# Kernel optimization log

Measured on AMD Instinct MI355X. Metric: run time of the kernel, lower is better.

The kernel has to match this reference:

```python
import jax, jax.numpy as jnp
import numpy as np

B, C, H, W = 4, 64, 128, 128
D_INNER, D_STATE, DT_RANK, K = 192, 16, 6, 4  # d_model = 3*C//2 = 96, expand = 2
EPS = 1e-5


def _haar():
    # pywt db1: dec_lo=[s,s], dec_hi=[-s,s]; code reverses dec_* and uses rec_* in
    # original order -> for Haar both dec and rec filter banks are identical.
    s = np.float32(1.0 / np.sqrt(2.0))
    lo = np.array([s, s], np.float32)
    hi = np.array([s, -s], np.float32)
    # stack order: [lo(i)lo(j), hi(i)lo(j), lo(i)hi(j), hi(i)hi(j)]
    return np.stack([np.outer(lo, lo), np.outer(hi, lo),
                     np.outer(lo, hi), np.outer(hi, hi)], 0)  # (4,2,2)

DEC = jnp.asarray(_haar())
REC = jnp.asarray(_haar())
DN = ('NCHW', 'OIHW', 'NCHW')


def _ln(x, s, b):
    m = x.mean(-1, keepdims=True)
    v = x.var(-1, keepdims=True)
    return (x - m) * jax.lax.rsqrt(v + EPS) * s + b


def _wt(x):
    b, c, h, w = x.shape
    wf = jnp.tile(DEC[:, None], (c, 1, 1, 1))  # (4c,1,2,2), groups=c, pad=0 for db1
    y = jax.lax.conv_general_dilated(x, wf, (2, 2), 'VALID',
                                     feature_group_count=c, dimension_numbers=DN)
    return y.reshape(b, c, 4, h // 2, w // 2)


def _iwt(x):
    # conv_transpose2d(stride=2, pad=0, groups=c) == lhs-dilated conv with flipped kernel, pad k-1
    b, c = x.shape[0], x.shape[1]
    h2, w2 = x.shape[3], x.shape[4]
    xr = x.reshape(b, c * 4, h2, w2)
    wf = jnp.tile(REC[:, ::-1, ::-1][None], (c, 1, 1, 1))  # (c,4,2,2)
    return jax.lax.conv_general_dilated(xr, wf, (1, 1), ((1, 1), (1, 1)),
                                        lhs_dilation=(2, 2), feature_group_count=c,
                                        dimension_numbers=DN)


def _ss2d(x, in_proj_w, conv_dw_w, conv_dw_b, x_proj_w, dt_proj_w, dt_proj_b,
          A_log, Ds, out_norm_s, out_norm_b, out_proj_w):
    b, d, h, w = x.shape  # d == D_INNER
    L = h * w
    xz = jnp.einsum('bchw,ec->behw', x, in_proj_w)  # (b,2d,h,w)
    x1, z = xz[:, :d], xz[:, d:]
    x1 = jax.lax.conv_general_dilated(x1, conv_dw_w, (1, 1), ((1, 1), (1, 1)),
                                      feature_group_count=d, dimension_numbers=DN)
    x1 = jax.nn.silu(x1 + conv_dw_b[None, :, None, None])
    # 4-direction flattening: hw, wh, and their reverses
    xf = x1.reshape(b, d, L)
    xt = x1.transpose(0, 1, 3, 2).reshape(b, d, L)
    xs = jnp.stack([xf, xt], 1)
    xs = jnp.concatenate([xs, xs[..., ::-1]], 1)  # (b,K,d,L)
    x_dbl = jnp.einsum('bkdl,kcd->bkcl', xs, x_proj_w)
    dts = x_dbl[:, :, :DT_RANK]
    Bs = x_dbl[:, :, DT_RANK:DT_RANK + D_STATE]   # (b,K,n,L)
    Cs = x_dbl[:, :, DT_RANK + D_STATE:]
    delta = jax.nn.softplus(jnp.einsum('bkrl,kdr->bkdl', dts, dt_proj_w)
                            + dt_proj_b[None, :, :, None])
    A = -jnp.exp(A_log)  # (K,d,n)

    def step(hc, inp):
        d_t, u_t, b_t, c_t = inp  # (b,K,d),(b,K,d),(b,K,n),(b,K,n)
        dA = jnp.exp(d_t[..., None] * A[None])
        hc = hc * dA + (d_t * u_t)[..., None] * b_t[:, :, None, :]
        y = jnp.einsum('bkdn,bkn->bkd', hc, c_t)
        return hc, y

    h0 = jnp.zeros((b, K, d, D_STATE), x.dtype)
    inputs = (delta.transpose(3, 0, 1, 2), xs.transpose(3, 0, 1, 2),
              Bs.transpose(3, 0, 1, 2), Cs.transpose(3, 0, 1, 2))
    _, ys = jax.lax.scan(step, h0, inputs)            # (L,b,K,d)
    out_y = ys.transpose(1, 2, 3, 0) + xs * Ds[None, :, :, None]  # (b,K,d,L)
    inv_y = out_y[:, 2:][..., ::-1]
    wh = out_y[:, 1].reshape(b, d, w, h).transpose(0, 1, 3, 2).reshape(b, d, L)
    invwh = inv_y[:, 1].reshape(b, d, w, h).transpose(0, 1, 3, 2).reshape(b, d, L)
    y = out_y[:, 0] + inv_y[:, 0] + wh + invwh        # (b,d,L)
    y = _ln(y.reshape(b, d, h, w).transpose(0, 2, 3, 1), out_norm_s, out_norm_b)
    y = y * jax.nn.silu(z.transpose(0, 2, 3, 1))
    y = jnp.einsum('bhwd,ed->bhwe', y, out_proj_w)
    return y.transpose(0, 3, 1, 2)


def reference(x, wt_low_scale, wt_high_scale, low_conv_w, in_proj_w, conv_dw_w,
              conv_dw_b, x_proj_w, dt_proj_w, dt_proj_b, A_log, Ds,
              out_norm_s, out_norm_b, out_proj_w, ln2_s, ln2_b, eca_w):
    b, c = x.shape[0], x.shape[1]
    wt = _wt(x)                                       # (b,c,4,h2,w2)
    h2, w2 = wt.shape[3], wt.shape[4]
    low = wt[:, :, 0] * wt_low_scale
    high = wt[:, :, 1:].reshape(b, c * 3, h2, w2) * wt_high_scale
    low = jax.nn.silu(jnp.einsum('bchw,ec->behw', low, low_conv_w[:, :, 0, 0]))
    high = _ss2d(high, in_proj_w, conv_dw_w, conv_dw_b, x_proj_w, dt_proj_w,
                 dt_proj_b, A_log, Ds, out_norm_s, out_norm_b, out_proj_w)
    high = _ln(high.transpose(0, 2, 3, 1), ln2_s, ln2_b).transpose(0, 3, 1, 2)
    mamba = jnp.tile(low, (1, 3, 1, 1)) * high
    merged = jnp.concatenate([low, mamba], 1).reshape(b, c, 4, h2, w2)
    y = _iwt(merged)                                  # (b,c,h,w)
    # ECA: gap -> conv1d(k=5) over channels -> sigmoid gate
    pooled = y.mean((2, 3))[:, None, :]               # (b,1,c)
    att = jax.lax.conv_general_dilated(pooled, eca_w.reshape(1, 1, 5), (1,),
                                       ((2, 2),), dimension_numbers=('NCH', 'OIH', 'NCH'))
    att = jax.nn.sigmoid(att[:, 0])
    return y * att[:, :, None, None] + x


def setup_inputs():
    key = jax.random.key(0)
    ks = jax.random.split(key, 20)
    f = jax.random.normal
    return {
        'x': f(ks[0], (B, C, H, W), jnp.float32),
        'wt_low_scale': jax.random.uniform(ks[1], (1, C, 1, 1), jnp.float32),
        'wt_high_scale': jax.random.uniform(ks[2], (1, 3 * C, 1, 1), jnp.float32),
        'low_conv_w': f(ks[3], (C, C, 1, 1), jnp.float32) * 0.1,
        'in_proj_w': f(ks[4], (2 * D_INNER, D_INNER), jnp.float32) * 0.05,
        'conv_dw_w': f(ks[5], (D_INNER, 1, 3, 3), jnp.float32) * 0.3,
        'conv_dw_b': f(ks[6], (D_INNER,), jnp.float32) * 0.1,
        'x_proj_w': f(ks[7], (K, DT_RANK + 2 * D_STATE, D_INNER), jnp.float32) * 0.05,
        'dt_proj_w': f(ks[8], (K, D_INNER, DT_RANK), jnp.float32) * 0.1,
        'dt_proj_b': jax.random.uniform(ks[9], (K, D_INNER), jnp.float32) - 4.0,
        'A_log': jax.random.uniform(ks[10], (K, D_INNER, D_STATE), jnp.float32),
        'Ds': f(ks[11], (K, D_INNER), jnp.float32) * 0.1,
        'out_norm_s': jnp.ones((D_INNER,), jnp.float32),
        'out_norm_b': jnp.zeros((D_INNER,), jnp.float32),
        'out_proj_w': f(ks[12], (D_INNER, D_INNER), jnp.float32) * 0.05,
        'ln2_s': jnp.ones((3 * C,), jnp.float32),
        'ln2_b': jnp.zeros((3 * C,), jnp.float32),
        'eca_w': f(ks[13], (5,), jnp.float32) * 0.3,
    }
```

## Files before the change

### kernel.cpp

```cpp
#include <hip/hip_runtime.h>

constexpr int cB = 4, cC = 64, cH = 128, cW = 128;
constexpr int cL = 4096;
constexpr int cD = 192, cN = 16;
constexpr int NCH = 64, CHUNK = 64;

__device__ __forceinline__ float silu_f(float v) { return v / (1.f + __expf(-v)); }

__global__ __launch_bounds__(256) void k_wt(const float* __restrict__ x,
                                            const float* __restrict__ wls,
                                            const float* __restrict__ whs,
                                            float* __restrict__ lraw,
                                            float* __restrict__ high) {
    int idx = blockIdx.x * 256 + threadIdx.x;
    int j = idx & 63, i = (idx >> 6) & 63, c = (idx >> 12) & 63, b = idx >> 18;
    const float* xp = x + (((size_t)(b * cC + c)) * cH + 2 * i) * cW + 2 * j;
    float x00 = xp[0], x01 = xp[1], x10 = xp[cW], x11 = xp[cW + 1];
    float s0 = 0.5f * (x00 + x01 + x10 + x11);
    float s1 = 0.5f * (x00 + x01 - x10 - x11);
    float s2 = 0.5f * (x00 - x01 + x10 - x11);
    float s3 = 0.5f * (x00 - x01 - x10 + x11);
    int l = i * 64 + j;
    lraw[(size_t)(b * cC + c) * cL + l] = s0 * wls[c];
    int ch = c * 3;
    high[(size_t)(b * cD + ch + 0) * cL + l] = s1 * whs[ch + 0];
    high[(size_t)(b * cD + ch + 1) * cL + l] = s2 * whs[ch + 1];
    high[(size_t)(b * cD + ch + 2) * cL + l] = s3 * whs[ch + 2];
}

__global__ __launch_bounds__(256) void k_lowconv(const float* __restrict__ lraw,
                                                 const float* __restrict__ w,
                                                 float* __restrict__ lowT) {
    int bid = blockIdx.x;
    int lt0 = (bid & 63) * 64;
    int b = bid >> 6;
    __shared__ float sW[16][68];
    __shared__ float sI[16][65];
    int tid = threadIdx.x, lt = tid & 63, eg = tid >> 6;
    float acc[16];
#pragma unroll
    for (int m = 0; m < 16; m++) acc[m] = 0.f;
    for (int c0 = 0; c0 < 64; c0 += 16) {
#pragma unroll
        for (int q = 0; q < 4; q++) {
            int tt = tid + q * 256;
            int cc = tt & 15, ee = tt >> 4;
            sW[cc][ee] = w[ee * 64 + c0 + cc];
        }
#pragma unroll
        for (int q = 0; q < 4; q++) {
            int tt = tid + q * 256;
            int ll = tt & 63, cc = tt >> 6;
            sI[cc][ll] = lraw[(size_t)(b * cC + c0 + cc) * cL + lt0 + ll];
        }
        __syncthreads();
#pragma unroll
        for (int cc = 0; cc < 16; cc++) {
            float iv = sI[cc][lt];
#pragma unroll
            for (int m = 0; m < 16; m++) acc[m] = fmaf(sW[cc][eg * 16 + m], iv, acc[m]);
        }
        __syncthreads();
    }
#pragma unroll
    for (int m = 0; m < 16; m++) {
        int e = eg * 16 + m;
        lowT[((size_t)b * cL + lt0 + lt) * 64 + e] = silu_f(acc[m]);
    }
}

__global__ __launch_bounds__(256) void k_inproj(const float* __restrict__ hi,
                                                const float* __restrict__ w,
                                                float* __restrict__ xout,
                                                float* __restrict__ zT) {
    int bid = blockIdx.x;
    int lt0 = (bid & 63) * 64;
    int et = (bid >> 6) % 6;
    int b = bid / (6 * 64);
    int e0 = et * 64;
    __shared__ float sW[16][68];
    __shared__ float sI[16][65];
    int tid = threadIdx.x, lt = tid & 63, eg = tid >> 6;
    float acc[16];
#pragma unroll
    for (int m = 0; m < 16; m++) acc[m] = 0.f;
    for (int c0 = 0; c0 < 192; c0 += 16) {
#pragma unroll
        for (int q = 0; q < 4; q++) {
            int tt = tid + q * 256;
            int cc = tt & 15, ee = tt >> 4;
            sW[cc][ee] = w[(e0 + ee) * 192 + c0 + cc];
        }
#pragma unroll
        for (int q = 0; q < 4; q++) {
            int tt = tid + q * 256;
            int ll = tt & 63, cc = tt >> 6;
            sI[cc][ll] = hi[(size_t)(b * cD + c0 + cc) * cL + lt0 + ll];
        }
        __syncthreads();
#pragma unroll
        for (int cc = 0; cc < 16; cc++) {
            float iv = sI[cc][lt];
#pragma unroll
            for (int m = 0; m < 16; m++) acc[m] = fmaf(sW[cc][eg * 16 + m], iv, acc[m]);
        }
        __syncthreads();
    }
#pragma unroll
    for (int m = 0; m < 16; m++) {
        int e = e0 + eg * 16 + m;
        float v = acc[m];
        if (e < 192) xout[(size_t)(b * cD + e) * cL + lt0 + lt] = v;
        else zT[((size_t)b * cL + lt0 + lt) * 192 + (e - 192)] = v;
    }
}

__global__ __launch_bounds__(256) void k_dwconv(const float* __restrict__ xin,
                                                const float* __restrict__ w,
                                                const float* __restrict__ bias,
                                                float* __restrict__ x1,
                                                float* __restrict__ u1) {
    int bd = blockIdx.x;
    int d = bd % cD;
    const float* xp = xin + (size_t)bd * cL;
    float wv[9];
#pragma unroll
    for (int t = 0; t < 9; t++) wv[t] = w[d * 9 + t];
    float bv = bias[d];
    __shared__ float sm[64][65];
    int tid = threadIdx.x;
#pragma unroll
    for (int q = 0; q < 16; q++) {
        int p = tid + q * 256;
        int i = p >> 6, j = p & 63;
        float acc = bv;
#pragma unroll
        for (int di = 0; di < 3; di++) {
            int ii = i + di - 1;
            if (ii < 0 || ii >= 64) continue;
#pragma unroll
            for (int dj = 0; dj < 3; dj++) {
                int jj = j + dj - 1;
                if (jj < 0 || jj >= 64) continue;
                acc = fmaf(wv[di * 3 + dj], xp[ii * 64 + jj], acc);
            }
        }
        sm[i][j] = silu_f(acc);
    }
    __syncthreads();
#pragma unroll
    for (int q = 0; q < 16; q++) {
        int p = tid + q * 256;
        x1[(size_t)bd * cL + p] = sm[p >> 6][p & 63];
        u1[(size_t)bd * cL + p] = sm[p & 63][p >> 6];
    }
}

__global__ __launch_bounds__(256) void k_xproj(const float* __restrict__ x1,
                                               const float* __restrict__ u1,
                                               const float* __restrict__ xpw,
                                               float* __restrict__ xdbl) {
    int bid = blockIdx.x;
    int lt0 = (bid & 63) * 64;
    int k = (bid >> 6) & 3;
    int b = bid >> 8;
    const float* src = (k & 1) ? u1 : x1;
    bool rev = (k >= 2);
    __shared__ float sW[16][68];
    __shared__ float sI[16][65];
    int tid = threadIdx.x, lt = tid & 63, eg = tid >> 6;
    float acc[16];
#pragma unroll
    for (int m = 0; m < 16; m++) acc[m] = 0.f;
    for (int c0 = 0; c0 < 192; c0 += 16) {
#pragma unroll
        for (int q = 0; q < 4; q++) {
            int tt = tid + q * 256;
            int cc = tt & 15, ee = tt >> 4;
            sW[cc][ee] = (ee < 38) ? xpw[(k * 38 + ee) * 192 + c0 + cc] : 0.f;
        }
#pragma unroll
        for (int q = 0; q < 4; q++) {
            int tt = tid + q * 256;
            int ll = tt & 63, cc = tt >> 6;
            int l = lt0 + ll;
            int lm = rev ? (cL - 1 - l) : l;
            sI[cc][ll] = src[(size_t)(b * cD + c0 + cc) * cL + lm];
        }
        __syncthreads();
#pragma unroll
        for (int cc = 0; cc < 16; cc++) {
            float iv = sI[cc][lt];
#pragma unroll
            for (int m = 0; m < 16; m++) acc[m] = fmaf(sW[cc][eg * 16 + m], iv, acc[m]);
        }
        __syncthreads();
    }
#pragma unroll
    for (int m = 0; m < 16; m++) {
        int e = eg * 16 + m;
        if (e < 38) xdbl[(size_t)((b * 4 + k) * 38 + e) * cL + lt0 + lt] = acc[m];
    }
}

__global__ __launch_bounds__(192) void k_scan1(const float* __restrict__ xdbl,
                                               const float* __restrict__ x1,
                                               const float* __restrict__ u1,
                                               const float* __restrict__ dtw,
                                               const float* __restrict__ dtb,
                                               const float* __restrict__ alog,
                                               float* __restrict__ P,
                                               float* __restrict__ S) {
    int bid = blockIdx.x;
    int ch = bid % NCH;
    int bk = bid / NCH;
    int k = bk & 3, b = bk >> 2;
    int d = threadIdx.x;
    float Av2[16], h[16], Pe[16];
#pragma unroll
    for (int n = 0; n < 16; n++) {
        Av2[n] = -__expf(alog[(k * 192 + d) * 16 + n]) * 1.44269504088896f;
        h[n] = 0.f;
        Pe[n] = 0.f;
    }
    float dtbv = dtb[k * 192 + d];
    float dtwv[6];
#pragma unroll
    for (int r = 0; r < 6; r++) dtwv[r] = dtw[(k * 192 + d) * 6 + r];
    const float* dtrows = xdbl + (size_t)(bk * 38) * cL;
    const float* Brow = xdbl + (size_t)(bk * 38 + 6) * cL;
    const float* usrc = ((k & 1) ? u1 : x1) + (size_t)b * cD * cL;
    bool rev = (k >= 2);

    __shared__ float su[192][17];
    __shared__ float sB[16][16];
    __shared__ float sdt[16][8];

    int col = d & 15, grp = d >> 4;
    int p0 = ch * CHUNK;
    for (int t0 = p0; t0 < p0 + CHUNK; t0 += 16) {
#pragma unroll
        for (int pp = 0; pp < 16; pp++) {
            int row = pp * 12 + grp;
            su[row][col] = usrc[(size_t)row * cL + (rev ? (cL - 1 - (t0 + col)) : (t0 + col))];
        }
        for (int idx = d; idx < 256; idx += 192) {
            sB[idx & 15][idx >> 4] = Brow[(size_t)(idx >> 4) * cL + t0 + (idx & 15)];
        }
        if (d < 96) sdt[col][grp] = dtrows[(size_t)grp * cL + t0 + col];
        __syncthreads();
#pragma unroll
        for (int l = 0; l < 16; l++) {
            float uv = su[d][l];
            float acc = dtbv;
#pragma unroll
            for (int r = 0; r < 6; r++) acc = fmaf(dtwv[r], sdt[l][r], acc);
            float sp = fmaxf(acc, 0.f) + __logf(1.f + __expf(-fabsf(acc)));
            float duB = sp * uv;
            float Bv[16];
            *reinterpret_cast<float4*>(&Bv[0])  = *reinterpret_cast<const float4*>(&sB[l][0]);
            *reinterpret_cast<float4*>(&Bv[4])  = *reinterpret_cast<const float4*>(&sB[l][4]);
            *reinterpret_cast<float4*>(&Bv[8])  = *reinterpret_cast<const float4*>(&sB[l][8]);
            *reinterpret_cast<float4*>(&Bv[12]) = *reinterpret_cast<const float4*>(&sB[l][12]);
#pragma unroll
            for (int n = 0; n < 16; n++) {
                float e = sp * Av2[n];
                Pe[n] += e;
                float dA = exp2f(e);
                h[n] = fmaf(h[n], dA, duB * Bv[n]);
            }
        }
        __syncthreads();
    }
    size_t base = (size_t)bid * 16 * 192 + d;
#pragma unroll
    for (int n = 0; n < 16; n++) {
        P[base + (size_t)n * 192] = exp2f(Pe[n]);
        S[base + (size_t)n * 192] = h[n];
    }
}

__global__ __launch_bounds__(256) void k_carry(const float* __restrict__ P,
                                               float* __restrict__ S) {
    int gid = blockIdx.x * 256 + threadIdx.x;
    int d = gid % 192;
    int n = (gid / 192) & 15;
    int bk = gid / 3072;
    float h = 0.f;
    for (int c = 0; c < NCH; c++) {
        size_t idx = ((size_t)(bk * NCH + c) * 16 + n) * 192 + d;
        h = fmaf(P[idx], h, S[idx]);
        S[idx] = h;
    }
}

__global__ __launch_bounds__(192) void k_scan2(const float* __restrict__ xdbl,
                                               const float* __restrict__ x1,
                                               const float* __restrict__ u1,
                                               const float* __restrict__ dtw,
                                               const float* __restrict__ dtb,
                                               const float* __restrict__ alog,
                                               const float* __restrict__ dss,
                                               const float* __restrict__ S,
                                               float* __restrict__ yacc) {
    int bid = blockIdx.x;
    int ch = bid % NCH;
    int bk = bid / NCH;
    int k = bk & 3, b = bk >> 2;
    int d = threadIdx.x;
    float Av2[16], h[16];
#pragma unroll
    for (int n = 0; n < 16; n++) {
        Av2[n] = -__expf(alog[(k * 192 + d) * 16 + n]) * 1.44269504088896f;
        h[n] = (ch == 0) ? 0.f : S[((size_t)(bk * NCH + ch - 1) * 16 + n) * 192 + d];
    }
    float Dv = dss[k * 192 + d];
    float dtbv = dtb[k * 192 + d];
    float dtwv[6];
#pragma unroll
    for (int r = 0; r < 6; r++) dtwv[r] = dtw[(k * 192 + d) * 6 + r];
    const float* dtrows = xdbl + (size_t)(bk * 38) * cL;
    const float* Brow = xdbl + (size_t)(bk * 38 + 6) * cL;
    const float* Crow = xdbl + (size_t)(bk * 38 + 22) * cL;
    const float* usrc = ((k & 1) ? u1 : x1) + (size_t)b * cD * cL;
    bool rev = (k >= 2);

    __shared__ float su[192][17];
    __shared__ float sB[16][16];
    __shared__ float sC[16][16];
    __shared__ float sdt[16][8];

    int col = d & 15, grp = d >> 4;
    int p0 = ch * CHUNK;
    for (int t0 = p0; t0 < p0 + CHUNK; t0 += 16) {
#pragma unroll
        for (int pp = 0; pp < 16; pp++) {
            int row = pp * 12 + grp;
            su[row][col] = usrc[(size_t)row * cL + (rev ? (cL - 1 - (t0 + col)) : (t0 + col))];
        }
        for (int idx = d; idx < 256; idx += 192) {
            sB[idx & 15][idx >> 4] = Brow[(size_t)(idx >> 4) * cL + t0 + (idx & 15)];
            sC[idx & 15][idx >> 4] = Crow[(size_t)(idx >> 4) * cL + t0 + (idx & 15)];
        }
        if (d < 96) sdt[col][grp] = dtrows[(size_t)grp * cL + t0 + col];
        __syncthreads();
#pragma unroll
        for (int l = 0; l < 16; l++) {
            float uv = su[d][l];
            float acc = dtbv;
#pragma unroll
            for (int r = 0; r < 6; r++) acc = fmaf(dtwv[r], sdt[l][r], acc);
            float sp = fmaxf(acc, 0.f) + __logf(1.f + __expf(-fabsf(acc)));
            float duB = sp * uv;
            float Bv[16], Cv[16];
            *reinterpret_cast<float4*>(&Bv[0])  = *reinterpret_cast<const float4*>(&sB[l][0]);
            *reinterpret_cast<float4*>(&Bv[4])  = *reinterpret_cast<const float4*>(&sB[l][4]);
            *reinterpret_cast<float4*>(&Bv[8])  = *reinterpret_cast<const float4*>(&sB[l][8]);
            *reinterpret_cast<float4*>(&Bv[12]) = *reinterpret_cast<const float4*>(&sB[l][12]);
            *reinterpret_cast<float4*>(&Cv[0])  = *reinterpret_cast<const float4*>(&sC[l][0]);
            *reinterpret_cast<float4*>(&Cv[4])  = *reinterpret_cast<const float4*>(&sC[l][4]);
            *reinterpret_cast<float4*>(&Cv[8])  = *reinterpret_cast<const float4*>(&sC[l][8]);
            *reinterpret_cast<float4*>(&Cv[12]) = *reinterpret_cast<const float4*>(&sC[l][12]);
            float y = uv * Dv;
#pragma unroll
            for (int n = 0; n < 16; n++) {
                float dA = exp2f(sp * Av2[n]);
                h[n] = fmaf(h[n], dA, duB * Bv[n]);
                y = fmaf(h[n], Cv[n], y);
            }
            int lg = t0 + l;
            int lm;
            if (k == 0) lm = lg;
            else if (k == 1) lm = (lg & 63) * 64 + (lg >> 6);
            else if (k == 2) lm = cL - 1 - lg;
            else { int q = cL - 1 - lg; lm = (q & 63) * 64 + (q >> 6); }
            atomicAdd(&yacc[((size_t)b * cL + lm) * 192 + d], y);
        }
        __syncthreads();
    }
}

__global__ __launch_bounds__(256) void k_comb(const float* __restrict__ yacc,
                                              const float* __restrict__ zT,
                                              const float* __restrict__ ons,
                                              const float* __restrict__ onb,
                                              float* __restrict__ yln) {
    int bid = blockIdx.x;
    int b = bid >> 10;
    int pg = bid & 1023;
    int tid = threadIdx.x;
    int wq = tid >> 6, lane = tid & 63;
    int l = pg * 4 + wq;
    float v[3];
    float s = 0.f, s2 = 0.f;
#pragma unroll
    for (int m = 0; m < 3; m++) {
        int d = lane + 64 * m;
        float t = yacc[((size_t)b * cL + l) * 192 + d];
        v[m] = t;
        s += t;
        s2 += t * t;
    }
#pragma unroll
    for (int o = 1; o < 64; o <<= 1) {
        s += __shfl_xor(s, o);
        s2 += __shfl_xor(s2, o);
    }
    float mean = s / 192.f;
    float var = s2 / 192.f - mean * mean;
    float rstd = rsqrtf(var + 1e-5f);
#pragma unroll
    for (int m = 0; m < 3; m++) {
        int d = lane + 64 * m;
        float zv = zT[((size_t)b * cL + l) * 192 + d];
        float yn = (v[m] - mean) * rstd * ons[d] + onb[d];
        yln[((size_t)b * cL + l) * 192 + d] = yn * silu_f(zv);
    }
}

__global__ __launch_bounds__(256) void k_outproj(const float* __restrict__ yln,
                                                 const float* __restrict__ w,
                                                 float* __restrict__ hout) {
    int bid = blockIdx.x;
    int lt0 = (bid & 63) * 64;
    int et = (bid >> 6) % 3;
    int b = bid / 192;
    int e0 = et * 64;
    __shared__ float sW[16][68];
    __shared__ float sI[16][65];
    int tid = threadIdx.x, lt = tid & 63, eg = tid >> 6;
    float acc[16];
#pragma unroll
    for (int m = 0; m < 16; m++) acc[m] = 0.f;
    for (int c0 = 0; c0 < 192; c0 += 16) {
#pragma unroll
        for (int q = 0; q < 4; q++) {
            int tt = tid + q * 256;
            int cc = tt & 15, ee = tt >> 4;
            sW[cc][ee] = w[(e0 + ee) * 192 + c0 + cc];
        }
#pragma unroll
        for (int q = 0; q < 4; q++) {
            int tt = tid + q * 256;
            int cc = tt & 15, lq = tt >> 4;
            sI[cc][lq] = yln[((size_t)b * cL + lt0 + lq) * 192 + c0 + cc];
        }
        __syncthreads();
#pragma unroll
        for (int cc = 0; cc < 16; cc++) {
            float iv = sI[cc][lt];
#pragma unroll
            for (int m = 0; m < 16; m++) acc[m] = fmaf(sW[cc][eg * 16 + m], iv, acc[m]);
        }
        __syncthreads();
    }
#pragma unroll
    for (int m = 0; m < 16; m++) {
        hout[((size_t)b * cL + lt0 + lt) * 192 + e0 + eg * 16 + m] = acc[m];
    }
}

__global__ __launch_bounds__(256) void k_ln2(const float* __restrict__ hout,
                                             const float* __restrict__ lowT,
                                             const float* __restrict__ l2s,
                                             const float* __restrict__ l2b,
                                             float* __restrict__ merged) {
    int bid = blockIdx.x;
    int b = bid >> 10;
    int pg = bid & 1023;
    int tid = threadIdx.x;
    int wq = tid >> 6, lane = tid & 63;
    int l = pg * 4 + wq;
    float v[3];
    float s = 0.f, s2 = 0.f;
#pragma unroll
    for (int m = 0; m < 3; m++) {
        int d = lane + 64 * m;
        float t = hout[((size_t)b * cL + l) * 192 + d];
        v[m] = t;
        s += t;
        s2 += t * t;
    }
#pragma unroll
    for (int o = 1; o < 64; o <<= 1) {
        s += __shfl_xor(s, o);
        s2 += __shfl_xor(s2, o);
    }
    float mean = s / 192.f;
    float var = s2 / 192.f - mean * mean;
    float rstd = rsqrtf(var + 1e-5f);
    float lv = lowT[((size_t)b * cL + l) * 64 + lane];
    float* mp = merged + ((size_t)b * cL + l) * 256;
    mp[lane] = lv;
#pragma unroll
    for (int m = 0; m < 3; m++) {
        int d = lane + 64 * m;
        float hn = (v[m] - mean) * rstd * l2s[d] + l2b[d];
        mp[64 + d] = lv * hn;
    }
}

__global__ __launch_bounds__(256) void k_iwt(const float* __restrict__ merged,
                                             float* __restrict__ ypre) {
    int idx = blockIdx.x * 256 + threadIdx.x;
    int j = idx & 63, i = (idx >> 6) & 63, g = (idx >> 12) & 63, b = idx >> 18;
    const float4 mv = *reinterpret_cast<const float4*>(merged + ((size_t)b * cL + i * 64 + j) * 256 + g * 4);
    float m0 = mv.x, m1 = mv.y, m2 = mv.z, m3 = mv.w;
    float* yp = ypre + ((size_t)(b * 64 + g) * cH + 2 * i) * cW + 2 * j;
    float2 r0 = make_float2(0.5f * (m0 + m1 + m2 + m3), 0.5f * (m0 + m1 - m2 - m3));
    float2 r1 = make_float2(0.5f * (m0 - m1 + m2 - m3), 0.5f * (m0 - m1 - m2 + m3));
    *reinterpret_cast<float2*>(yp) = r0;
    *reinterpret_cast<float2*>(yp + cW) = r1;
}

__global__ __launch_bounds__(256) void k_pool(const float* __restrict__ ypre,
                                              float* __restrict__ pooled) {
    int bg = blockIdx.x;
    const float* p = ypre + (size_t)bg * (cH * cW);
    float s = 0.f;
    for (int t = threadIdx.x; t < cH * cW; t += 256) s += p[t];
#pragma unroll
    for (int o = 1; o < 64; o <<= 1) s += __shfl_xor(s, o);
    __shared__ float red[4];
    if ((threadIdx.x & 63) == 0) red[threadIdx.x >> 6] = s;
    __syncthreads();
    if (threadIdx.x == 0) pooled[bg] = (red[0] + red[1] + red[2] + red[3]) * (1.f / (cH * cW));
}

__global__ __launch_bounds__(256) void k_eca(const float* __restrict__ pooled,
                                             const float* __restrict__ w,
                                             float* __restrict__ att) {
    int t = threadIdx.x;
    int b = t >> 6, c = t & 63;
    float s = 0.f;
#pragma unroll
    for (int u = 0; u < 5; u++) {
        int cc = c + u - 2;
        if (cc >= 0 && cc < 64) s += w[u] * pooled[b * 64 + cc];
    }
    att[t] = 1.f / (1.f + __expf(-s));
}

__global__ __launch_bounds__(256) void k_final(const float* __restrict__ ypre,
                                               const float* __restrict__ x,
                                               const float* __restrict__ att,
                                               float* __restrict__ out) {
    int idx = blockIdx.x * 256 + threadIdx.x;
    size_t base = (size_t)idx * 4;
    int bc = (int)(base >> 14);
    float a = att[bc];
    float4 yv = *reinterpret_cast<const float4*>(ypre + base);
    float4 xv = *reinterpret_cast<const float4*>(x + base);
    float4 o;
    o.x = fmaf(yv.x, a, xv.x);
    o.y = fmaf(yv.y, a, xv.y);
    o.z = fmaf(yv.z, a, xv.z);
    o.w = fmaf(yv.w, a, xv.w);
    *reinterpret_cast<float4*>(out + base) = o;
}

extern "C" void kernel_launch(void* const* d_in, const int* in_sizes, int n_in,
                              void* d_out, int out_size, void* d_ws, size_t ws_size,
                              hipStream_t stream) {
    const float* x    = (const float*)d_in[0];
    const float* wls  = (const float*)d_in[1];
    const float* whs  = (const float*)d_in[2];
    const float* lcw  = (const float*)d_in[3];
    const float* ipw  = (const float*)d_in[4];
    const float* dww  = (const float*)d_in[5];
    const float* dwb  = (const float*)d_in[6];
    const float* xpw  = (const float*)d_in[7];
    const float* dtw  = (const float*)d_in[8];
    const float* dtb  = (const float*)d_in[9];
    const float* alog = (const float*)d_in[10];
    const float* dss  = (const float*)d_in[11];
    const float* ons  = (const float*)d_in[12];
    const float* onb  = (const float*)d_in[13];
    const float* opw  = (const float*)d_in[14];
    const float* l2s  = (const float*)d_in[15];
    const float* l2b  = (const float*)d_in[16];
    const float* ecw  = (const float*)d_in[17];
    float* out = (float*)d_out;
    float* w = (float*)d_ws;

    float* high   = w + 0;
    float* lraw   = w + 3145728;
    float* lowT   = w + 4194304;
    float* xbuf   = w + 5242880;
    float* zT     = w + 8388608;
    float* x1     = w + 11534336;
    float* u1     = w + 14680064;
    float* yacc   = w + 17825792;
    float* Sbuf   = w + 20971520;
    float* xdbl   = high;
    float* Pbuf   = xbuf;
    float* yln    = xbuf;
    float* hout   = high;
    float* merged = x1;
    float* ypre   = yacc;
    float* pooled = lraw;
    float* att    = lraw + 256;

    k_wt<<<4096, 256, 0, stream>>>(x, wls, whs, lraw, high);
    k_lowconv<<<256, 256, 0, stream>>>(lraw, lcw, lowT);
    k_inproj<<<1536, 256, 0, stream>>>(high, ipw, xbuf, zT);
    k_dwconv<<<768, 256, 0, stream>>>(xbuf, dww, dwb, x1, u1);
    k_xproj<<<1024, 256, 0, stream>>>(x1, u1, xpw, xdbl);
    hipMemsetAsync(yacc, 0, (size_t)cB * cL * cD * sizeof(float), stream);
    k_scan1<<<1024, 192, 0, stream>>>(xdbl, x1, u1, dtw, dtb, alog, Pbuf, Sbuf);
    k_carry<<<192, 256, 0, stream>>>(Pbuf, Sbuf);
    k_scan2<<<1024, 192, 0, stream>>>(xdbl, x1, u1, dtw, dtb, alog, dss, Sbuf, yacc);
    k_comb<<<4096, 256, 0, stream>>>(yacc, zT, ons, onb, yln);
    k_outproj<<<768, 256, 0, stream>>>(yln, opw, hout);
    k_ln2<<<4096, 256, 0, stream>>>(hout, lowT, l2s, l2b, merged);
    k_iwt<<<4096, 256, 0, stream>>>(merged, ypre);
    k_pool<<<256, 256, 0, stream>>>(ypre, pooled);
    k_eca<<<1, 256, 0, stream>>>(pooled, ecw, att);
    k_final<<<4096, 256, 0, stream>>>(ypre, x, att, out);
}
```

Measured before the change: 441.6 us.

## Split scan state dimension across two thread halves in chunked selective scan

Both scan kernels now launch 384 threads per block, with each thread owning 8 of the 16 state entries for one channel instead of all 16. This doubles the threads available to hide the serial exp/fma recurrence latency and halves per-thread register arrays. In exchange, the softplus/dt computation is duplicated across both halves, and scan2 now issues twice as many atomicAdds into yacc, one partial sum per half.

```diff
diff --git a/kernel.cpp b/kernel.cpp
--- a/kernel.cpp
+++ b/kernel.cpp
@@ -203,7 +203,7 @@
     }
 }
 
-__global__ __launch_bounds__(192) void k_scan1(const float* __restrict__ xdbl,
+__global__ __launch_bounds__(384) void k_scan1(const float* __restrict__ xdbl,
                                                const float* __restrict__ x1,
                                                const float* __restrict__ u1,
                                                const float* __restrict__ dtw,
@@ -215,13 +215,15 @@
     int ch = bid % NCH;
     int bk = bid / NCH;
     int k = bk & 3, b = bk >> 2;
-    int d = threadIdx.x;
-    float Av2[16], h[16], Pe[16];
-#pragma unroll
-    for (int n = 0; n < 16; n++) {
-        Av2[n] = -__expf(alog[(k * 192 + d) * 16 + n]) * 1.44269504088896f;
-        h[n] = 0.f;
-        Pe[n] = 0.f;
+    int tid = threadIdx.x;
+    int d = tid % 192, nh = tid / 192;
+    int n0 = nh * 8;
+    float Av2[8], h[8], Pe[8];
+#pragma unroll
+    for (int j = 0; j < 8; j++) {
+        Av2[j] = -__expf(alog[(k * 192 + d) * 16 + n0 + j]) * 1.44269504088896f;
+        h[j] = 0.f;
+        Pe[j] = 0.f;
     }
     float dtbv = dtb[k * 192 + d];
     float dtwv[6];
@@ -236,18 +238,16 @@
     __shared__ float sB[16][16];
     __shared__ float sdt[16][8];
 
-    int col = d & 15, grp = d >> 4;
     int p0 = ch * CHUNK;
     for (int t0 = p0; t0 < p0 + CHUNK; t0 += 16) {
 #pragma unroll
-        for (int pp = 0; pp < 16; pp++) {
-            int row = pp * 12 + grp;
+        for (int pp = 0; pp < 8; pp++) {
+            int row = pp * 24 + (tid >> 4);
+            int col = tid & 15;
             su[row][col] = usrc[(size_t)row * cL + (rev ? (cL - 1 - (t0 + col)) : (t0 + col))];
         }
-        for (int idx = d; idx < 256; idx += 192) {
-            sB[idx & 15][idx >> 4] = Brow[(size_t)(idx >> 4) * cL + t0 + (idx & 15)];
-        }
-        if (d < 96) sdt[col][grp] = dtrows[(size_t)grp * cL + t0 + col];
+        if (tid < 256) sB[tid & 15][tid >> 4] = Brow[(size_t)(tid >> 4) * cL + t0 + (tid & 15)];
+        if (tid < 96) sdt[tid & 15][tid >> 4] = dtrows[(size_t)(tid >> 4) * cL + t0 + (tid & 15)];
         __syncthreads();
 #pragma unroll
         for (int l = 0; l < 16; l++) {
@@ -257,26 +257,24 @@
             for (int r = 0; r < 6; r++) acc = fmaf(dtwv[r], sdt[l][r], acc);
             float sp = fmaxf(acc, 0.f) + __logf(1.f + __expf(-fabsf(acc)));
             float duB = sp * uv;
-            float Bv[16];
-            *reinterpret_cast<float4*>(&Bv[0])  = *reinterpret_cast<const float4*>(&sB[l][0]);
-            *reinterpret_cast<float4*>(&Bv[4])  = *reinterpret_cast<const float4*>(&sB[l][4]);
-            *reinterpret_cast<float4*>(&Bv[8])  = *reinterpret_cast<const float4*>(&sB[l][8]);
-            *reinterpret_cast<float4*>(&Bv[12]) = *reinterpret_cast<const float4*>(&sB[l][12]);
-#pragma unroll
-            for (int n = 0; n < 16; n++) {
-                float e = sp * Av2[n];
-                Pe[n] += e;
+            float Bv[8];
+            *reinterpret_cast<float4*>(&Bv[0]) = *reinterpret_cast<const float4*>(&sB[l][n0]);
+            *reinterpret_cast<float4*>(&Bv[4]) = *reinterpret_cast<const float4*>(&sB[l][n0 + 4]);
+#pragma unroll
+            for (int j = 0; j < 8; j++) {
+                float e = sp * Av2[j];
+                Pe[j] += e;
                 float dA = exp2f(e);
-                h[n] = fmaf(h[n], dA, duB * Bv[n]);
+                h[j] = fmaf(h[j], dA, duB * Bv[j]);
             }
         }
         __syncthreads();
     }
     size_t base = (size_t)bid * 16 * 192 + d;
 #pragma unroll
-    for (int n = 0; n < 16; n++) {
-        P[base + (size_t)n * 192] = exp2f(Pe[n]);
-        S[base + (size_t)n * 192] = h[n];
+    for (int j = 0; j < 8; j++) {
+        P[base + (size_t)(n0 + j) * 192] = exp2f(Pe[j]);
+        S[base + (size_t)(n0 + j) * 192] = h[j];
     }
 }
 
@@ -294,7 +292,7 @@
     }
 }
 
-__global__ __launch_bounds__(192) void k_scan2(const float* __restrict__ xdbl,
+__global__ __launch_bounds__(384) void k_scan2(const float* __restrict__ xdbl,
                                                const float* __restrict__ x1,
                                                const float* __restrict__ u1,
                                                const float* __restrict__ dtw,
@@ -307,12 +305,14 @@
     int ch = bid % NCH;
     int bk = bid / NCH;
     int k = bk & 3, b = bk >> 2;
-    int d = threadIdx.x;
-    float Av2[16], h[16];
-#pragma unroll
-    for (int n = 0; n < 16; n++) {
-        Av2[n] = -__expf(alog[(k * 192 + d) * 16 + n]) * 1.44269504088896f;
-        h[n] = (ch == 0) ? 0.f : S[((size_t)(bk * NCH + ch - 1) * 16 + n) * 192 + d];
+    int tid = threadIdx.x;
+    int d = tid % 192, nh = tid / 192;
+    int n0 = nh * 8;
+    float Av2[8], h[8];
+#pragma unroll
+    for (int j = 0; j < 8; j++) {
+        Av2[j] = -__expf(alog[(k * 192 + d) * 16 + n0 + j]) * 1.44269504088896f;
+        h[j] = (ch == 0) ? 0.f : S[((size_t)(bk * NCH + ch - 1) * 16 + n0 + j) * 192 + d];
     }
     float Dv = dss[k * 192 + d];
     float dtbv = dtb[k * 192 + d];
@@ -330,19 +330,19 @@
     __shared__ float sC[16][16];
     __shared__ float sdt[16][8];
 
-    int col = d & 15, grp = d >> 4;
     int p0 = ch * CHUNK;
     for (int t0 = p0; t0 < p0 + CHUNK; t0 += 16) {
 #pragma unroll
-        for (int pp = 0; pp < 16; pp++) {
-            int row = pp * 12 + grp;
+        for (int pp = 0; pp < 8; pp++) {
+            int row = pp * 24 + (tid >> 4);
+            int col = tid & 15;
             su[row][col] = usrc[(size_t)row * cL + (rev ? (cL - 1 - (t0 + col)) : (t0 + col))];
         }
-        for (int idx = d; idx < 256; idx += 192) {
-            sB[idx & 15][idx >> 4] = Brow[(size_t)(idx >> 4) * cL + t0 + (idx & 15)];
-            sC[idx & 15][idx >> 4] = Crow[(size_t)(idx >> 4) * cL + t0 + (idx & 15)];
-        }
-        if (d < 96) sdt[col][grp] = dtrows[(size_t)grp * cL + t0 + col];
+        if (tid < 256) {
+            sB[tid & 15][tid >> 4] = Brow[(size_t)(tid >> 4) * cL + t0 + (tid & 15)];
+            sC[tid & 15][tid >> 4] = Crow[(size_t)(tid >> 4) * cL + t0 + (tid & 15)];
+        }
+        if (tid < 96) sdt[tid & 15][tid >> 4] = dtrows[(size_t)(tid >> 4) * cL + t0 + (tid & 15)];
         __syncthreads();
 #pragma unroll
         for (int l = 0; l < 16; l++) {
@@ -352,21 +352,17 @@
             for (int r = 0; r < 6; r++) acc = fmaf(dtwv[r], sdt[l][r], acc);
             float sp = fmaxf(acc, 0.f) + __logf(1.f + __expf(-fabsf(acc)));
             float duB = sp * uv;
-            float Bv[16], Cv[16];
-            *reinterpret_cast<float4*>(&Bv[0])  = *reinterpret_cast<const float4*>(&sB[l][0]);
-            *reinterpret_cast<float4*>(&Bv[4])  = *reinterpret_cast<const float4*>(&sB[l][4]);
-            *reinterpret_cast<float4*>(&Bv[8])  = *reinterpret_cast<const float4*>(&sB[l][8]);
-            *reinterpret_cast<float4*>(&Bv[12]) = *reinterpret_cast<const float4*>(&sB[l][12]);
-            *reinterpret_cast<float4*>(&Cv[0])  = *reinterpret_cast<const float4*>(&sC[l][0]);
-            *reinterpret_cast<float4*>(&Cv[4])  = *reinterpret_cast<const float4*>(&sC[l][4]);
-            *reinterpret_cast<float4*>(&Cv[8])  = *reinterpret_cast<const float4*>(&sC[l][8]);
-            *reinterpret_cast<float4*>(&Cv[12]) = *reinterpret_cast<const float4*>(&sC[l][12]);
-            float y = uv * Dv;
-#pragma unroll
-            for (int n = 0; n < 16; n++) {
-                float dA = exp2f(sp * Av2[n]);
-                h[n] = fmaf(h[n], dA, duB * Bv[n]);
-                y = fmaf(h[n], Cv[n], y);
+            float Bv[8], Cv[8];
+            *reinterpret_cast<float4*>(&Bv[0]) = *reinterpret_cast<const float4*>(&sB[l][n0]);
+            *reinterpret_cast<float4*>(&Bv[4]) = *reinterpret_cast<const float4*>(&sB[l][n0 + 4]);
+            *reinterpret_cast<float4*>(&Cv[0]) = *reinterpret_cast<const float4*>(&sC[l][n0]);
+            *reinterpret_cast<float4*>(&Cv[4]) = *reinterpret_cast<const float4*>(&sC[l][n0 + 4]);
+            float y = (nh == 0) ? uv * Dv : 0.f;
+#pragma unroll
+            for (int j = 0; j < 8; j++) {
+                float dA = exp2f(sp * Av2[j]);
+                h[j] = fmaf(h[j], dA, duB * Bv[j]);
+                y = fmaf(h[j], Cv[j], y);
             }
             int lg = t0 + l;
             int lm;
@@ -607,9 +603,9 @@
     k_dwconv<<<768, 256, 0, stream>>>(xbuf, dww, dwb, x1, u1);
     k_xproj<<<1024, 256, 0, stream>>>(x1, u1, xpw, xdbl);
     hipMemsetAsync(yacc, 0, (size_t)cB * cL * cD * sizeof(float), stream);
-    k_scan1<<<1024, 192, 0, stream>>>(xdbl, x1, u1, dtw, dtb, alog, Pbuf, Sbuf);
+    k_scan1<<<1024, 384, 0, stream>>>(xdbl, x1, u1, dtw, dtb, alog, Pbuf, Sbuf);
     k_carry<<<192, 256, 0, stream>>>(Pbuf, Sbuf);
-    k_scan2<<<1024, 192, 0, stream>>>(xdbl, x1, u1, dtw, dtb, alog, dss, Sbuf, yacc);
+    k_scan2<<<1024, 384, 0, stream>>>(xdbl, x1, u1, dtw, dtb, alog, dss, Sbuf, yacc);
     k_comb<<<4096, 256, 0, stream>>>(yacc, zT, ons, onb, yln);
     k_outproj<<<768, 256, 0, stream>>>(yln, opw, hout);
     k_ln2<<<4096, 256, 0, stream>>>(hout, lowT, l2s, l2b, merged);
```

Result: slower. 455.3 us (+3.1%).

## Double-buffer scan B/C/dt tiles, load u directly into registers, sum dt once

Applied to the files above, without the earlier changes.

Both selective-scan kernels now double-buffer the B, C and dt tiles in shared memory. The next 16-step tile is prefetched while the current one is processed, so one barrier per tile is dropped. The u values are read straight from global memory into registers as float4 vectors instead of going through a 192x17 shared tile. scan1 builds the chunk decay from one accumulated sum of dt (exp2(A*sum dt)) rather than 16 per-state running sums, scan2 splits the C dot product into two independent accumulators, and the in_proj block index is reordered so the six e-tiles sharing an input tile run next to each other. The risks are per-thread strided float4 loads with poor coalescing across d, and slightly different floating-point rounding.

```diff
diff --git a/kernel.cpp b/kernel.cpp
--- a/kernel.cpp
+++ b/kernel.cpp
@@ -74,9 +74,10 @@
                                                 float* __restrict__ xout,
                                                 float* __restrict__ zT) {
     int bid = blockIdx.x;
-    int lt0 = (bid & 63) * 64;
-    int et = (bid >> 6) % 6;
-    int b = bid / (6 * 64);
+    int et = bid % 6;
+    int blt = bid / 6;
+    int lt0 = (blt & 63) * 64;
+    int b = blt >> 6;
     int e0 = et * 64;
     __shared__ float sW[16][68];
     __shared__ float sI[16][65];
@@ -215,13 +216,13 @@
     int ch = bid % NCH;
     int bk = bid / NCH;
     int k = bk & 3, b = bk >> 2;
-    int d = threadIdx.x;
-    float Av2[16], h[16], Pe[16];
-#pragma unroll
-    for (int n = 0; n < 16; n++) {
-        Av2[n] = -__expf(alog[(k * 192 + d) * 16 + n]) * 1.44269504088896f;
-        h[n] = 0.f;
-        Pe[n] = 0.f;
+    int tid = threadIdx.x;
+    int d = tid;
+    float Av2[16], h[16];
+#pragma unroll
+    for (int j = 0; j < 16; j++) {
+        Av2[j] = -__expf(alog[(k * 192 + d) * 16 + j]) * 1.44269504088896f;
+        h[j] = 0.f;
     }
     float dtbv = dtb[k * 192 + d];
     float dtwv[6];
@@ -229,54 +230,61 @@
     for (int r = 0; r < 6; r++) dtwv[r] = dtw[(k * 192 + d) * 6 + r];
     const float* dtrows = xdbl + (size_t)(bk * 38) * cL;
     const float* Brow = xdbl + (size_t)(bk * 38 + 6) * cL;
-    const float* usrc = ((k & 1) ? u1 : x1) + (size_t)b * cD * cL;
+    const float* ubase = ((k & 1) ? u1 : x1) + ((size_t)b * cD + d) * cL;
     bool rev = (k >= 2);
 
-    __shared__ float su[192][17];
-    __shared__ float sB[16][16];
-    __shared__ float sdt[16][8];
-
-    int col = d & 15, grp = d >> 4;
+    __shared__ float sB[2][16][16];
+    __shared__ float sdt[2][16][8];
+
+    int rowA = tid >> 4, colA = tid & 15;
     int p0 = ch * CHUNK;
+
+    for (int idx = tid; idx < 256; idx += 192)
+        sB[0][idx & 15][idx >> 4] = Brow[(size_t)(idx >> 4) * cL + p0 + (idx & 15)];
+    if (tid < 96) sdt[0][colA][rowA] = dtrows[(size_t)rowA * cL + p0 + colA];
+
+    float Q = 0.f;
+    int cur = 0;
     for (int t0 = p0; t0 < p0 + CHUNK; t0 += 16) {
-#pragma unroll
-        for (int pp = 0; pp < 16; pp++) {
-            int row = pp * 12 + grp;
-            su[row][col] = usrc[(size_t)row * cL + (rev ? (cL - 1 - (t0 + col)) : (t0 + col))];
-        }
-        for (int idx = d; idx < 256; idx += 192) {
-            sB[idx & 15][idx >> 4] = Brow[(size_t)(idx >> 4) * cL + t0 + (idx & 15)];
-        }
-        if (d < 96) sdt[col][grp] = dtrows[(size_t)grp * cL + t0 + col];
-        __syncthreads();
+        __syncthreads();
+        if (t0 + 16 < p0 + CHUNK) {
+            int t1 = t0 + 16;
+            for (int idx = tid; idx < 256; idx += 192)
+                sB[cur ^ 1][idx & 15][idx >> 4] = Brow[(size_t)(idx >> 4) * cL + t1 + (idx & 15)];
+            if (tid < 96) sdt[cur ^ 1][colA][rowA] = dtrows[(size_t)rowA * cL + t1 + colA];
+        }
+        float uvals[16];
+        {
+            const float* up = rev ? (ubase + (cL - 16 - t0)) : (ubase + t0);
+#pragma unroll
+            for (int q = 0; q < 4; q++)
+                *reinterpret_cast<float4*>(&uvals[q * 4]) = *reinterpret_cast<const float4*>(up + q * 4);
+        }
 #pragma unroll
         for (int l = 0; l < 16; l++) {
-            float uv = su[d][l];
             float acc = dtbv;
 #pragma unroll
-            for (int r = 0; r < 6; r++) acc = fmaf(dtwv[r], sdt[l][r], acc);
+            for (int r = 0; r < 6; r++) acc = fmaf(dtwv[r], sdt[cur][l][r], acc);
             float sp = fmaxf(acc, 0.f) + __logf(1.f + __expf(-fabsf(acc)));
+            Q += sp;
+            float uv = rev ? uvals[15 - l] : uvals[l];
             float duB = sp * uv;
             float Bv[16];
-            *reinterpret_cast<float4*>(&Bv[0])  = *reinterpret_cast<const float4*>(&sB[l][0]);
-            *reinterpret_cast<float4*>(&Bv[4])  = *reinterpret_cast<const float4*>(&sB[l][4]);
-            *reinterpret_cast<float4*>(&Bv[8])  = *reinterpret_cast<const float4*>(&sB[l][8]);
-            *reinterpret_cast<float4*>(&Bv[12]) = *reinterpret_cast<const float4*>(&sB[l][12]);
-#pragma unroll
-            for (int n = 0; n < 16; n++) {
-                float e = sp * Av2[n];
-                Pe[n] += e;
-                float dA = exp2f(e);
-                h[n] = fmaf(h[n], dA, duB * Bv[n]);
-            }
-        }
-        __syncthreads();
+            *reinterpret_cast<float4*>(&Bv[0])  = *reinterpret_cast<const float4*>(&sB[cur][l][0]);
+            *reinterpret_cast<float4*>(&Bv[4])  = *reinterpret_cast<const float4*>(&sB[cur][l][4]);
+            *reinterpret_cast<float4*>(&Bv[8])  = *reinterpret_cast<const float4*>(&sB[cur][l][8]);
+            *reinterpret_cast<float4*>(&Bv[12]) = *reinterpret_cast<const float4*>(&sB[cur][l][12]);
+#pragma unroll
+            for (int j = 0; j < 16; j++)
+                h[j] = fmaf(h[j], exp2f(sp * Av2[j]), duB * Bv[j]);
+        }
+        cur ^= 1;
     }
     size_t base = (size_t)bid * 16 * 192 + d;
 #pragma unroll
-    for (int n = 0; n < 16; n++) {
-        P[base + (size_t)n * 192] = exp2f(Pe[n]);
-        S[base + (size_t)n * 192] = h[n];
+    for (int j = 0; j < 16; j++) {
+        P[base + (size_t)j * 192] = exp2f(Av2[j] * Q);
+        S[base + (size_t)j * 192] = h[j];
     }
 }
 
@@ -307,12 +315,13 @@
     int ch = bid % NCH;
     int bk = bid / NCH;
     int k = bk & 3, b = bk >> 2;
-    int d = threadIdx.x;
+    int tid = threadIdx.x;
+    int d = tid;
     float Av2[16], h[16];
 #pragma unroll
-    for (int n = 0; n < 16; n++) {
-        Av2[n] = -__expf(alog[(k * 192 + d) * 16 + n]) * 1.44269504088896f;
-        h[n] = (ch == 0) ? 0.f : S[((size_t)(bk * NCH + ch - 1) * 16 + n) * 192 + d];
+    for (int j = 0; j < 16; j++) {
+        Av2[j] = -__expf(alog[(k * 192 + d) * 16 + j]) * 1.44269504088896f;
+        h[j] = (ch == 0) ? 0.f : S[((size_t)(bk * NCH + ch - 1) * 16 + j) * 192 + d];
     }
     float Dv = dss[k * 192 + d];
     float dtbv = dtb[k * 192 + d];
@@ -322,61 +331,78 @@
     const float* dtrows = xdbl + (size_t)(bk * 38) * cL;
     const float* Brow = xdbl + (size_t)(bk * 38 + 6) * cL;
     const float* Crow = xdbl + (size_t)(bk * 38 + 22) * cL;
-    const float* usrc = ((k & 1) ? u1 : x1) + (size_t)b * cD * cL;
+    const float* ubase = ((k & 1) ? u1 : x1) + ((size_t)b * cD + d) * cL;
     bool rev = (k >= 2);
 
-    __shared__ float su[192][17];
-    __shared__ float sB[16][16];
-    __shared__ float sC[16][16];
-    __shared__ float sdt[16][8];
-
-    int col = d & 15, grp = d >> 4;
+    __shared__ float sB[2][16][16];
+    __shared__ float sC[2][16][16];
+    __shared__ float sdt[2][16][8];
+
+    int rowA = tid >> 4, colA = tid & 15;
     int p0 = ch * CHUNK;
+
+    for (int idx = tid; idx < 256; idx += 192) {
+        sB[0][idx & 15][idx >> 4] = Brow[(size_t)(idx >> 4) * cL + p0 + (idx & 15)];
+        sC[0][idx & 15][idx >> 4] = Crow[(size_t)(idx >> 4) * cL + p0 + (idx & 15)];
+    }
+    if (tid < 96) sdt[0][colA][rowA] = dtrows[(size_t)rowA * cL + p0 + colA];
+
+    int cur = 0;
     for (int t0 = p0; t0 < p0 + CHUNK; t0 += 16) {
-#pragma unroll
-        for (int pp = 0; pp < 16; pp++) {
-            int row = pp * 12 + grp;
-            su[row][col] = usrc[(size_t)row * cL + (rev ? (cL - 1 - (t0 + col)) : (t0 + col))];
-        }
-        for (int idx = d; idx < 256; idx += 192) {
-            sB[idx & 15][idx >> 4] = Brow[(size_t)(idx >> 4) * cL + t0 + (idx & 15)];
-            sC[idx & 15][idx >> 4] = Crow[(size_t)(idx >> 4) * cL + t0 + (idx & 15)];
-        }
-        if (d < 96) sdt[col][grp] = dtrows[(size_t)grp * cL + t0 + col];
-        __syncthreads();
+        __syncthreads();
+        if (t0 + 16 < p0 + CHUNK) {
+            int t1 = t0 + 16;
+            for (int idx = tid; idx < 256; idx += 192) {
+                sB[cur ^ 1][idx & 15][idx >> 4] = Brow[(size_t)(idx >> 4) * cL + t1 + (idx & 15)];
+                sC[cur ^ 1][idx & 15][idx >> 4] = Crow[(size_t)(idx >> 4) * cL + t1 + (idx & 15)];
+            }
+            if (tid < 96) sdt[cur ^ 1][colA][rowA] = dtrows[(size_t)rowA * cL + t1 + colA];
+        }
+        float uvals[16];
+        {
+            const float* up = rev ? (ubase + (cL - 16 - t0)) : (ubase + t0);
+#pragma unroll
+            for (int q = 0; q < 4; q++)
+                *reinterpret_cast<float4*>(&uvals[q * 4]) = *reinterpret_cast<const float4*>(up + q * 4);
+        }
 #pragma unroll
         for (int l = 0; l < 16; l++) {
-            float uv = su[d][l];
             float acc = dtbv;
 #pragma unroll
-            for (int r = 0; r < 6; r++) acc = fmaf(dtwv[r], sdt[l][r], acc);
+            for (int r = 0; r < 6; r++) acc = fmaf(dtwv[r], sdt[cur][l][r], acc);
             float sp = fmaxf(acc, 0.f) + __logf(1.f + __expf(-fabsf(acc)));
+            float uv = rev ? uvals[15 - l] : uvals[l];
             float duB = sp * uv;
             float Bv[16], Cv[16];
-            *reinterpret_cast<float4*>(&Bv[0])  = *reinterpret_cast<const float4*>(&sB[l][0]);
-            *reinterpret_cast<float4*>(&Bv[4])  = *reinterpret_cast<const float4*>(&sB[l][4]);
-            *reinterpret_cast<float4*>(&Bv[8])  = *reinterpret_cast<const float4*>(&sB[l][8]);
-            *reinterpret_cast<float4*>(&Bv[12]) = *reinterpret_cast<const float4*>(&sB[l][12]);
-            *reinterpret_cast<float4*>(&Cv[0])  = *reinterpret_cast<const float4*>(&sC[l][0]);
-            *reinterpret_cast<float4*>(&Cv[4])  = *reinterpret_cast<const float4*>(&sC[l][4]);
-            *reinterpret_cast<float4*>(&Cv[8])  = *reinterpret_cast<const float4*>(&sC[l][8]);
-            *reinterpret_cast<float4*>(&Cv[12]) = *reinterpret_cast<const float4*>(&sC[l][12]);
-            float y = uv * Dv;
-#pragma unroll
-            for (int n = 0; n < 16; n++) {
-                float dA = exp2f(sp * Av2[n]);
-                h[n] = fmaf(h[n], dA, duB * Bv[n]);
-                y = fmaf(h[n], Cv[n], y);
+            *reinterpret_cast<float4*>(&Bv[0])  = *reinterpret_cast<const float4*>(&sB[cur][l][0]);
+            *reinterpret_cast<float4*>(&Bv[4])  = *reinterpret_cast<const float4*>(&sB[cur][l][4]);
+            *reinterpret_cast<float4*>(&Bv[8])  = *reinterpret_cast<const float4*>(&sB[cur][l][8]);
+            *reinterpret_cast<float4*>(&Bv[12]) = *reinterpret_cast<const float4*>(&sB[cur][l][12]);
+            *reinterpret_cast<float4*>(&Cv[0])  = *reinterpret_cast<const float4*>(&sC[cur][l][0]);
+            *reinterpret_cast<float4*>(&Cv[4])  = *reinterpret_cast<const float4*>(&sC[cur][l][4]);
+            *reinterpret_cast<float4*>(&Cv[8])  = *reinterpret_cast<const float4*>(&sC[cur][l][8]);
+            *reinterpret_cast<float4*>(&Cv[12]) = *reinterpret_cast<const float4*>(&sC[cur][l][12]);
+            float yA = 0.f, yB = 0.f;
+#pragma unroll
+            for (int j = 0; j < 8; j++) {
+                h[j] = fmaf(h[j], exp2f(sp * Av2[j]), duB * Bv[j]);
+                yA = fmaf(h[j], Cv[j], yA);
             }
+#pragma unroll
+            for (int j = 8; j < 16; j++) {
+                h[j] = fmaf(h[j], exp2f(sp * Av2[j]), duB * Bv[j]);
+                yB = fmaf(h[j], Cv[j], yB);
+            }
+            float y = yA + yB + uv * Dv;
             int lg = t0 + l;
             int lm;
             if (k == 0) lm = lg;
             else if (k == 1) lm = (lg & 63) * 64 + (lg >> 6);
             else if (k == 2) lm = cL - 1 - lg;
-            else { int q = cL - 1 - lg; lm = (q & 63) * 64 + (q >> 6); }
+            else { int qq = cL - 1 - lg; lm = (qq & 63) * 64 + (qq >> 6); }
             atomicAdd(&yacc[((size_t)b * cL + lm) * 192 + d], y);
         }
-        __syncthreads();
+        cur ^= 1;
     }
 }
 
```

Result: faster. 414.3 us, median of 5 (-6.2%).
